# Optimization experiments

Hardware: AMD Instinct MI355X
Metric: run time of the kernel (lower is better)

Reference implementation:

```python
import jax, jax.numpy as jnp
import numpy as np

NUM_NODES_G1 = 60000
NUM_NODES_G2 = 50000
NUM_REL = 16
NUM_BASES = 4
DIM = 128  # node_dim == hidden_dim == final_dim
L_COMMON = 100


def _concept_layer(x, edge_index):
    # Gather-based concept propagation: x_i <- x_i + mean_{j in N(i)} x_j
    src, dst = edge_index[0], edge_index[1]
    n = x.shape[0]
    agg = jax.ops.segment_sum(x[src], dst, num_segments=n)
    deg = jax.ops.segment_sum(jnp.ones((src.shape[0],), x.dtype), dst, num_segments=n)
    return x + agg / jnp.clip(deg, 1.0)[:, None]


def _rgcn_layer(x, edge_index, edge_type, basis, comp, root, bias):
    # Basis-decomposed RGCN: out_i = x_i @ root + bias + sum_r (1/|N_i^r|) sum_{j in N_i^r} x_j @ W_r,
    # W_r = sum_b comp[r,b] * basis[b]. Reorder: scatter comp-weighted x[src] per basis, then one GEMM per basis.
    src, dst = edge_index[0], edge_index[1]
    n = x.shape[0]
    e = src.shape[0]
    seg = dst * NUM_REL + edge_type  # per-(node, relation) bucket
    cnt = jax.ops.segment_sum(jnp.ones((e,), x.dtype), seg, num_segments=n * NUM_REL)
    norm = 1.0 / jnp.clip(cnt, 1.0)
    coef = comp[edge_type] * norm[seg][:, None]  # [E, B]
    xsrc = x[src]  # [E, D] -- dominant gather traffic
    out = x @ root + bias
    for b in range(NUM_BASES):  # small fixed loop over bases
        agg_b = jax.ops.segment_sum(xsrc * coef[:, b:b + 1], dst, num_segments=n)
        out = out + agg_b @ basis[b]
    return out


def setup_inputs() -> dict:
    key = jax.random.key(0)
    ks = jax.random.split(key, 16)
    e2, e1 = 800000, 800000
    return {
        "edge_index_g2": jax.random.randint(ks[0], (2, e2), 0, NUM_NODES_G2),
        "edge_type_g2": jax.random.randint(ks[1], (e2,), 0, NUM_REL),
        "edge_index_g1": jax.random.randint(ks[2], (2, e1), 0, NUM_NODES_G1),
        "left_common": jax.random.randint(ks[3], (L_COMMON,), 0, NUM_NODES_G1),
        "all_node_embedding": jax.random.normal(ks[4], (NUM_NODES_G1, DIM), jnp.float32),
        "basis1": jax.random.normal(ks[5], (NUM_BASES, DIM, DIM), jnp.float32) * 0.05,
        "comp1": jax.random.normal(ks[6], (NUM_REL, NUM_BASES), jnp.float32),
        "root1": jax.random.normal(ks[7], (DIM, DIM), jnp.float32) * 0.05,
        "bias1": jnp.zeros((DIM,), jnp.float32),
        "basis2": jax.random.normal(ks[8], (NUM_BASES, DIM, DIM), jnp.float32) * 0.05,
        "comp2": jax.random.normal(ks[9], (NUM_REL, NUM_BASES), jnp.float32),
        "root2": jax.random.normal(ks[10], (DIM, DIM), jnp.float32) * 0.05,
        "bias2": jnp.zeros((DIM,), jnp.float32),
        "weights": jax.random.uniform(ks[11], (DIM, 1), jnp.float32),
    }


def reference(edge_index_g2, edge_type_g2, edge_index_g1, left_common,
              all_node_embedding, basis1, comp1, root1, bias1,
              basis2, comp2, root2, bias2, weights):
    x_g1 = jax.nn.relu(_concept_layer(all_node_embedding, edge_index_g1))
    x = x_g1[:NUM_NODES_G2]
    x = _rgcn_layer(x, edge_index_g2, edge_type_g2, basis1, comp1, root1, bias1)
    x = jax.nn.relu(x)  # relu_use == 1
    x_g2 = _rgcn_layer(x, edge_index_g2, edge_type_g2, basis2, comp2, root2, bias2)
    ty = x_g1[left_common]  # [L, D]
    # mul_def outer elementwise product followed by matmul with weights collapses to one contraction:
    # logits[n,l] = sum_d x_g2[n,d] * ty[l,d] * w[d]
    logits = jnp.einsum('nd,ld,d->nl', x_g2, ty, weights[:, 0])
    return jax.nn.softmax(logits, axis=1)
```

## Files before the change

kernel.cpp:

```cpp
#include <hip/hip_runtime.h>
#include <hip/hip_bf16.h>
#include <math.h>

#define N1 60000
#define N2 50000
#define DIM 128
#define NREL 16
#define NB 4
#define LCOM 100
#define LPAD 112

typedef __attribute__((ext_vector_type(8))) short short8;
typedef __attribute__((ext_vector_type(4))) float f32x4;

__device__ __forceinline__ float bf2f(unsigned short u) {
    union { unsigned int i; float f; } c; c.i = ((unsigned int)u) << 16; return c.f;
}
__device__ __forceinline__ unsigned short f2bf(float f) {
    union { float f; unsigned int i; } c; c.f = f;
    unsigned int r = c.i + 0x7FFF + ((c.i >> 16) & 1);
    return (unsigned short)(r >> 16);
}
__device__ __forceinline__ void split8(float4 a, float4 b, short8& h, short8& l) {
    float f[8] = {a.x, a.y, a.z, a.w, b.x, b.y, b.z, b.w};
#pragma unroll
    for (int j = 0; j < 8; j++) {
        unsigned short hh = f2bf(f[j]);
        h[j] = (short)hh;
        l[j] = (short)f2bf(f[j] - bf2f(hh));
    }
}

__global__ void k_prep_w(const float* __restrict__ root, const float* __restrict__ basis,
                         unsigned short* __restrict__ Wh, unsigned short* __restrict__ Wl) {
    int t = blockIdx.x * blockDim.x + threadIdx.x;
    if (t >= 640 * 128) return;
    int k = t >> 7, n = t & 127;
    float v = (k < 128) ? root[k * 128 + n] : basis[(k - 128) * 128 + n];
    unsigned short h = f2bf(v);
    Wh[n * 640 + k] = h;
    Wl[n * 640 + k] = f2bf(v - bf2f(h));
}

__global__ void k_hist_deg(const int* __restrict__ ei, int* __restrict__ deg, int E) {
    int e = blockIdx.x * blockDim.x + threadIdx.x;
    if (e >= E) return;
    atomicAdd(deg + ei[E + e], 1);
}

__global__ void k_hist_dt(const int* __restrict__ ei, const int* __restrict__ et,
                          int* __restrict__ cnt, int E) {
    int e = blockIdx.x * blockDim.x + threadIdx.x;
    if (e >= E) return;
    atomicAdd(cnt + ei[E + e] * NREL + et[e], 1);
}

__global__ void k_deg_from_cnt(const int* __restrict__ cnt, int* __restrict__ deg, int n) {
    int i = blockIdx.x * blockDim.x + threadIdx.x;
    if (i >= n) return;
    int s = 0;
#pragma unroll
    for (int t = 0; t < NREL; t++) s += cnt[i * NREL + t];
    deg[i] = s;
}

__global__ __launch_bounds__(256) void k_scan_p1(const int* __restrict__ in,
                                                 int* __restrict__ bsum, int n) {
    __shared__ int red[256];
    int base = blockIdx.x * 1024;
    int tid = threadIdx.x;
    int s = 0;
#pragma unroll
    for (int j = 0; j < 4; j++) {
        int i = base + tid * 4 + j;
        if (i < n) s += in[i];
    }
    red[tid] = s;
    __syncthreads();
    for (int d = 128; d; d >>= 1) {
        if (tid < d) red[tid] += red[tid + d];
        __syncthreads();
    }
    if (tid == 0) bsum[blockIdx.x] = red[0];
}

__global__ __launch_bounds__(64) void k_scan_p2(const int* __restrict__ bsum,
                                                int* __restrict__ boff,
                                                int* __restrict__ off, int nb, int n) {
    __shared__ int s[64];
    int tid = threadIdx.x;
    int v = (tid < nb) ? bsum[tid] : 0;
    s[tid] = v;
    __syncthreads();
    for (int d = 1; d < 64; d <<= 1) {
        int t = (tid >= d) ? s[tid - d] : 0;
        __syncthreads();
        s[tid] += t;
        __syncthreads();
    }
    if (tid < nb) boff[tid] = s[tid] - v;
    if (tid == 63) off[n] = s[63];
}

__global__ __launch_bounds__(256) void k_scan_p3(const int* __restrict__ in,
                                                 const int* __restrict__ boff,
                                                 int* __restrict__ off,
                                                 int* __restrict__ cur, int n) {
    __shared__ int red[256];
    int base = blockIdx.x * 1024;
    int tid = threadIdx.x;
    int v[4];
    int s = 0;
#pragma unroll
    for (int j = 0; j < 4; j++) {
        int i = base + tid * 4 + j;
        v[j] = (i < n) ? in[i] : 0;
        s += v[j];
    }
    red[tid] = s;
    __syncthreads();
    for (int d = 1; d < 256; d <<= 1) {
        int t = (tid >= d) ? red[tid - d] : 0;
        __syncthreads();
        red[tid] += t;
        __syncthreads();
    }
    int run = boff[blockIdx.x] + red[tid] - s;
#pragma unroll
    for (int j = 0; j < 4; j++) {
        int i = base + tid * 4 + j;
        if (i < n) {
            off[i] = run; cur[i] = run;
            run += v[j];
        }
    }
}

__global__ void k_csr_scatter1(const int* __restrict__ ei, int* __restrict__ cur,
                               int* __restrict__ elist, int E) {
    int e = blockIdx.x * blockDim.x + threadIdx.x;
    if (e >= E) return;
    int pos = atomicAdd(cur + ei[E + e], 1);
    elist[pos] = ei[e];
}

__global__ void k_csr_scatter2(const int* __restrict__ ei, const int* __restrict__ et,
                               const int* __restrict__ cnt, int* __restrict__ cur,
                               int* __restrict__ elist, float* __restrict__ nrmv, int E) {
    int e = blockIdx.x * blockDim.x + threadIdx.x;
    if (e >= E) return;
    int dst = ei[E + e], t = et[e];
    int pos = atomicAdd(cur + dst, 1);
    elist[pos] = (ei[e] << 4) | t;
    nrmv[pos] = 1.0f / fmaxf((float)cnt[dst * NREL + t], 1.0f);
}

__global__ __launch_bounds__(256) void k_concept_gather(const float* __restrict__ emb,
                                                        const int* __restrict__ off,
                                                        const int* __restrict__ elist,
                                                        float* __restrict__ xg1, int n) {
    int node = blockIdx.x * 4 + (threadIdx.x >> 6);
    int lane = threadIdx.x & 63;
    if (node >= n) return;
    int half = lane >> 5, d4 = (lane & 31) * 4;
    int s0 = off[node], s1 = off[node + 1];
    float4 acc = {0.f, 0.f, 0.f, 0.f};
    int i = s0;
    for (; i + 4 <= s1; i += 4) {
        int sa = elist[i + half];
        int sb = elist[i + 2 + half];
        float4 va = *(const float4*)(emb + (size_t)sa * DIM + d4);
        float4 vb = *(const float4*)(emb + (size_t)sb * DIM + d4);
        acc.x += va.x + vb.x; acc.y += va.y + vb.y;
        acc.z += va.z + vb.z; acc.w += va.w + vb.w;
    }
    for (; i < s1; i += 2) {
        int e = i + half;
        bool ok = e < s1;
        int s = elist[ok ? e : i];
        float4 v = *(const float4*)(emb + (size_t)s * DIM + d4);
        if (ok) { acc.x += v.x; acc.y += v.y; acc.z += v.z; acc.w += v.w; }
    }
    acc.x += __shfl_xor(acc.x, 32, 64);
    acc.y += __shfl_xor(acc.y, 32, 64);
    acc.z += __shfl_xor(acc.z, 32, 64);
    acc.w += __shfl_xor(acc.w, 32, 64);
    if (half == 0) {
        float inv = 1.0f / (float)max(s1 - s0, 1);
        float4 e = *(const float4*)(emb + (size_t)node * DIM + d4);
        float4 o = {fmaxf(e.x + acc.x * inv, 0.f), fmaxf(e.y + acc.y * inv, 0.f),
                    fmaxf(e.z + acc.z * inv, 0.f), fmaxf(e.w + acc.w * inv, 0.f)};
        *(float4*)(xg1 + (size_t)node * DIM + d4) = o;
    }
}

__global__ __launch_bounds__(64) void k_tyw(const float* __restrict__ emb,
                                            const int* __restrict__ off,
                                            const int* __restrict__ elist,
                                            const int* __restrict__ lc,
                                            const float* __restrict__ w,
                                            unsigned short* __restrict__ tyh,
                                            unsigned short* __restrict__ tyl) {
    int l = blockIdx.x;
    int lane = threadIdx.x;
    int d0 = lane * 2;
    if (l >= LCOM) {
        ushort2 z = {0, 0};
        *(ushort2*)(tyh + (size_t)l * 128 + d0) = z;
        *(ushort2*)(tyl + (size_t)l * 128 + d0) = z;
        return;
    }
    int row = lc[l];
    int s0 = off[row], s1 = off[row + 1];
    float2 acc = {0.f, 0.f};
    for (int i = s0; i < s1; i++) {
        int s = elist[i];
        float2 v = *(const float2*)(emb + (size_t)s * DIM + lane * 2);
        acc.x += v.x; acc.y += v.y;
    }
    float inv = 1.0f / (float)max(s1 - s0, 1);
    float2 e = *(const float2*)(emb + (size_t)row * DIM + lane * 2);
    float v0 = fmaxf(e.x + acc.x * inv, 0.f) * w[d0];
    float v1 = fmaxf(e.y + acc.y * inv, 0.f) * w[d0 + 1];
    unsigned short h0 = f2bf(v0), h1 = f2bf(v1);
    ushort2 hh = {h0, h1};
    ushort2 ll = {f2bf(v0 - bf2f(h0)), f2bf(v1 - bf2f(h1))};
    *(ushort2*)(tyh + (size_t)l * 128 + d0) = hh;
    *(ushort2*)(tyl + (size_t)l * 128 + d0) = ll;
}

__global__ __launch_bounds__(256) void k_rgcn_gather(const float* __restrict__ x,
                                                     const int* __restrict__ off,
                                                     const int* __restrict__ elist,
                                                     const float* __restrict__ nrmv,
                                                     const float* __restrict__ comp,
                                                     float* __restrict__ agg, int n) {
    __shared__ float scomp[NREL * NB];
    if (threadIdx.x < NREL * NB) scomp[threadIdx.x] = comp[threadIdx.x];
    __syncthreads();
    int node = blockIdx.x * 4 + (threadIdx.x >> 6);
    int lane = threadIdx.x & 63;
    if (node >= n) return;
    int half = lane >> 5, d4 = (lane & 31) * 4;
    int s0 = off[node], s1 = off[node + 1];
    float4 a0 = {0, 0, 0, 0}, a1 = a0, a2 = a0, a3 = a0;
    int i = s0;
#define RG_EDGE(E_IDX, NRM)                                                    \
    {                                                                          \
        int p = elist[E_IDX];                                                  \
        float nr = (NRM);                                                      \
        int s = p >> 4, t = p & 15;                                            \
        float4 cf = *(const float4*)(scomp + t * 4);                           \
        float4 v = *(const float4*)(x + (size_t)s * DIM + d4);                 \
        float c0 = cf.x * nr, c1 = cf.y * nr, c2 = cf.z * nr, c3 = cf.w * nr;  \
        a0.x = fmaf(c0, v.x, a0.x); a0.y = fmaf(c0, v.y, a0.y);                \
        a0.z = fmaf(c0, v.z, a0.z); a0.w = fmaf(c0, v.w, a0.w);                \
        a1.x = fmaf(c1, v.x, a1.x); a1.y = fmaf(c1, v.y, a1.y);                \
        a1.z = fmaf(c1, v.z, a1.z); a1.w = fmaf(c1, v.w, a1.w);                \
        a2.x = fmaf(c2, v.x, a2.x); a2.y = fmaf(c2, v.y, a2.y);                \
        a2.z = fmaf(c2, v.z, a2.z); a2.w = fmaf(c2, v.w, a2.w);                \
        a3.x = fmaf(c3, v.x, a3.x); a3.y = fmaf(c3, v.y, a3.y);                \
        a3.z = fmaf(c3, v.z, a3.z); a3.w = fmaf(c3, v.w, a3.w);                \
    }
    for (; i + 4 <= s1; i += 4) {
        RG_EDGE(i + half, nrmv[i + half]);
        RG_EDGE(i + 2 + half, nrmv[i + 2 + half]);
    }
    for (; i < s1; i += 2) {
        int e = i + half;
        bool ok = e < s1;
        int ei_ = ok ? e : i;
        RG_EDGE(ei_, ok ? nrmv[ei_] : 0.0f);
    }
#undef RG_EDGE
    a0.x += __shfl_xor(a0.x, 32, 64); a0.y += __shfl_xor(a0.y, 32, 64);
    a0.z += __shfl_xor(a0.z, 32, 64); a0.w += __shfl_xor(a0.w, 32, 64);
    a1.x += __shfl_xor(a1.x, 32, 64); a1.y += __shfl_xor(a1.y, 32, 64);
    a1.z += __shfl_xor(a1.z, 32, 64); a1.w += __shfl_xor(a1.w, 32, 64);
    a2.x += __shfl_xor(a2.x, 32, 64); a2.y += __shfl_xor(a2.y, 32, 64);
    a2.z += __shfl_xor(a2.z, 32, 64); a2.w += __shfl_xor(a2.w, 32, 64);
    a3.x += __shfl_xor(a3.x, 32, 64); a3.y += __shfl_xor(a3.y, 32, 64);
    a3.z += __shfl_xor(a3.z, 32, 64); a3.w += __shfl_xor(a3.w, 32, 64);
    if (half == 0) {
        float* o = agg + (size_t)node * (NB * DIM) + d4;
        *(float4*)(o + 0 * DIM) = a0;
        *(float4*)(o + 1 * DIM) = a1;
        *(float4*)(o + 2 * DIM) = a2;
        *(float4*)(o + 3 * DIM) = a3;
    }
}

#define LDSK 40
__global__ __launch_bounds__(256) void k_gemm(const float* __restrict__ x,
                                              const float* __restrict__ agg,
                                              const unsigned short* __restrict__ Wh,
                                              const unsigned short* __restrict__ Wl,
                                              const float* __restrict__ bias,
                                              float* __restrict__ out, int relu) {
    __shared__ __align__(16) short Ah[128 * LDSK];
    __shared__ __align__(16) short Al[128 * LDSK];
    __shared__ __align__(16) short Bh[128 * LDSK];
    __shared__ __align__(16) short Bl[128 * LDSK];
    int tid = threadIdx.x;
    int lane = tid & 63, wid = tid >> 6;
    int wave_m = wid >> 1, wave_n = wid & 1;
    int l15 = lane & 15, quad = lane >> 4;
    int row0 = blockIdx.x * 128;

    int srow = tid >> 1, skh = (tid & 1) * 16;

    f32x4 acc[4][4] = {};
    for (int k0 = 0; k0 < 640; k0 += 32) {
        {
            int rg = row0 + srow;
            float4 q0 = {0, 0, 0, 0}, q1 = q0, q2 = q0, q3 = q0;
            if (rg < N2) {
                const float* src = (k0 < 128) ? (x + (size_t)rg * 128 + k0 + skh)
                                              : (agg + (size_t)rg * 512 + (k0 - 128) + skh);
                q0 = *(const float4*)(src + 0);
                q1 = *(const float4*)(src + 4);
                q2 = *(const float4*)(src + 8);
                q3 = *(const float4*)(src + 12);
            }
            short8 h0, l0, h1, l1;
            split8(q0, q1, h0, l0);
            split8(q2, q3, h1, l1);
            *(short8*)(&Ah[srow * LDSK + skh]) = h0;
            *(short8*)(&Ah[srow * LDSK + skh + 8]) = h1;
            *(short8*)(&Al[srow * LDSK + skh]) = l0;
            *(short8*)(&Al[srow * LDSK + skh + 8]) = l1;
        }
        {
            const unsigned short* sh = Wh + (size_t)srow * 640 + k0 + skh;
            const unsigned short* sl = Wl + (size_t)srow * 640 + k0 + skh;
            *(short8*)(&Bh[srow * LDSK + skh]) = *(const short8*)(sh);
            *(short8*)(&Bh[srow * LDSK + skh + 8]) = *(const short8*)(sh + 8);
            *(short8*)(&Bl[srow * LDSK + skh]) = *(const short8*)(sl);
            *(short8*)(&Bl[srow * LDSK + skh + 8]) = *(const short8*)(sl + 8);
        }
        __syncthreads();
        short8 ah[4], al[4], bh[4], bl[4];
#pragma unroll
        for (int i = 0; i < 4; i++) {
            int ro = (wave_m * 64 + i * 16 + l15) * LDSK + quad * 8;
            ah[i] = *(const short8*)(&Ah[ro]);
            al[i] = *(const short8*)(&Al[ro]);
        }
#pragma unroll
        for (int j = 0; j < 4; j++) {
            int ro = (wave_n * 64 + j * 16 + l15) * LDSK + quad * 8;
            bh[j] = *(const short8*)(&Bh[ro]);
            bl[j] = *(const short8*)(&Bl[ro]);
        }
#pragma unroll
        for (int i = 0; i < 4; i++)
#pragma unroll
            for (int j = 0; j < 4; j++) {
                acc[i][j] = __builtin_amdgcn_mfma_f32_16x16x32_bf16(al[i], bh[j], acc[i][j], 0, 0, 0);
                acc[i][j] = __builtin_amdgcn_mfma_f32_16x16x32_bf16(ah[i], bl[j], acc[i][j], 0, 0, 0);
                acc[i][j] = __builtin_amdgcn_mfma_f32_16x16x32_bf16(ah[i], bh[j], acc[i][j], 0, 0, 0);
            }
        __syncthreads();
    }
#pragma unroll
    for (int j = 0; j < 4; j++) {
        int gcol = wave_n * 64 + j * 16 + l15;
        float bv = bias[gcol];
#pragma unroll
        for (int i = 0; i < 4; i++) {
            int grow_base = row0 + wave_m * 64 + i * 16 + quad * 4;
#pragma unroll
            for (int r = 0; r < 4; r++) {
                int grow = grow_base + r;
                if (grow >= N2) continue;
                float v = acc[i][j][r] + bv;
                if (relu) v = fmaxf(v, 0.f);
                out[(size_t)grow * 128 + gcol] = v;
            }
        }
    }
}

__global__ __launch_bounds__(256) void k_logits(const float* __restrict__ h2,
                                                const unsigned short* __restrict__ tyh,
                                                const unsigned short* __restrict__ tyl,
                                                float* __restrict__ out, int M) {
    int wid = threadIdx.x >> 6, lane = threadIdx.x & 63;
    int l15 = lane & 15, quad = lane >> 4;
    int row0w = blockIdx.x * 64 + wid * 16;
    int arow = min(row0w + l15, M - 1);
    f32x4 acc[7] = {};
#pragma unroll
    for (int k0 = 0; k0 < 128; k0 += 32) {
        const float* ap = h2 + (size_t)arow * 128 + k0 + quad * 8;
        float4 q0 = *(const float4*)(ap);
        float4 q1 = *(const float4*)(ap + 4);
        short8 ah, al;
        split8(q0, q1, ah, al);
#pragma unroll
        for (int j = 0; j < 7; j++) {
            size_t bo = (size_t)(j * 16 + l15) * 128 + k0 + quad * 8;
            short8 bh = *(const short8*)(tyh + bo);
            short8 bl = *(const short8*)(tyl + bo);
            acc[j] = __builtin_amdgcn_mfma_f32_16x16x32_bf16(al, bh, acc[j], 0, 0, 0);
            acc[j] = __builtin_amdgcn_mfma_f32_16x16x32_bf16(ah, bl, acc[j], 0, 0, 0);
            acc[j] = __builtin_amdgcn_mfma_f32_16x16x32_bf16(ah, bh, acc[j], 0, 0, 0);
        }
    }
    bool v6 = (l15 < LCOM - 96);
#pragma unroll
    for (int r = 0; r < 4; r++) {
        int grow = row0w + quad * 4 + r;
        float m = -INFINITY;
#pragma unroll
        for (int j = 0; j < 6; j++) m = fmaxf(m, acc[j][r]);
        if (v6) m = fmaxf(m, acc[6][r]);
        m = fmaxf(m, __shfl_xor(m, 8, 64));
        m = fmaxf(m, __shfl_xor(m, 4, 64));
        m = fmaxf(m, __shfl_xor(m, 2, 64));
        m = fmaxf(m, __shfl_xor(m, 1, 64));
        float e[7];
        float s = 0.f;
#pragma unroll
        for (int j = 0; j < 6; j++) { e[j] = __expf(acc[j][r] - m); s += e[j]; }
        e[6] = v6 ? __expf(acc[6][r] - m) : 0.f;
        s += e[6];
        s += __shfl_xor(s, 8, 64);
        s += __shfl_xor(s, 4, 64);
        s += __shfl_xor(s, 2, 64);
        s += __shfl_xor(s, 1, 64);
        float inv = 1.0f / s;
        if (grow < M) {
#pragma unroll
            for (int j = 0; j < 6; j++) out[(size_t)grow * LCOM + j * 16 + l15] = e[j] * inv;
            if (v6) out[(size_t)grow * LCOM + 96 + l15] = e[6] * inv;
        }
    }
}

extern "C" void kernel_launch(void* const* d_in, const int* in_sizes, int n_in,
                              void* d_out, int out_size, void* d_ws, size_t ws_size,
                              hipStream_t stream) {
    const int* ei2 = (const int*)d_in[0];
    const int* et2 = (const int*)d_in[1];
    const int* ei1 = (const int*)d_in[2];
    const int* lc = (const int*)d_in[3];
    const float* emb = (const float*)d_in[4];
    const float* basis1 = (const float*)d_in[5];
    const float* comp1 = (const float*)d_in[6];
    const float* root1 = (const float*)d_in[7];
    const float* bias1 = (const float*)d_in[8];
    const float* basis2 = (const float*)d_in[9];
    const float* comp2 = (const float*)d_in[10];
    const float* root2 = (const float*)d_in[11];
    const float* bias2 = (const float*)d_in[12];
    const float* wts = (const float*)d_in[13];
    float* out = (float*)d_out;
    int E2 = in_sizes[0] / 2, E1 = in_sizes[2] / 2;

    float* ws = (float*)d_ws;
    float* xg1 = ws;
    float* h1 = xg1 + 6400000;
    float* agg = h1 + 6400000;
    float* nrmv = agg + 25600000;
    unsigned short* tyh = (unsigned short*)(nrmv + 800000);
    unsigned short* tyl = tyh + LPAD * 128;
    unsigned short* Wh1 = tyl + LPAD * 128;
    unsigned short* Wl1 = Wh1 + 81920;
    unsigned short* Wh2 = Wl1 + 81920;
    unsigned short* Wl2 = Wh2 + 81920;
    int* ipool = (int*)(Wl2 + 81920);
    int* deg1 = ipool;
    int* off1 = deg1 + 60000;
    int* cur1 = off1 + 60001;
    int* elist1 = cur1 + 60000;
    int* cnt2 = elist1 + 800000;
    int* deg2 = cnt2 + 800000;
    int* off2 = deg2 + 50000;
    int* cur2 = off2 + 50001;
    int* elist2 = cur2 + 50000;
    int* bsum1 = elist2 + 800000;
    int* boff1 = bsum1 + 64;
    int* bsum2 = boff1 + 64;
    int* boff2 = bsum2 + 64;
    float* h2 = xg1;

    const int NB1 = (N1 + 1023) / 1024;
    const int NB2 = (N2 + 1023) / 1024;

    k_prep_w<<<(640 * 128 + 255) / 256, 256, 0, stream>>>(root1, basis1, Wh1, Wl1);
    k_prep_w<<<(640 * 128 + 255) / 256, 256, 0, stream>>>(root2, basis2, Wh2, Wl2);

    hipMemsetAsync(deg1, 0, 60000 * sizeof(int), stream);
    k_hist_deg<<<(E1 + 255) / 256, 256, 0, stream>>>(ei1, deg1, E1);
    k_scan_p1<<<NB1, 256, 0, stream>>>(deg1, bsum1, N1);
    k_scan_p2<<<1, 64, 0, stream>>>(bsum1, boff1, off1, NB1, N1);
    k_scan_p3<<<NB1, 256, 0, stream>>>(deg1, boff1, off1, cur1, N1);
    k_csr_scatter1<<<(E1 + 255) / 256, 256, 0, stream>>>(ei1, cur1, elist1, E1);
    k_concept_gather<<<(N2 + 3) / 4, 256, 0, stream>>>(emb, off1, elist1, xg1, N2);
    k_tyw<<<LPAD, 64, 0, stream>>>(emb, off1, elist1, lc, wts, tyh, tyl);

    hipMemsetAsync(cnt2, 0, 800000 * sizeof(int), stream);
    k_hist_dt<<<(E2 + 255) / 256, 256, 0, stream>>>(ei2, et2, cnt2, E2);
    k_deg_from_cnt<<<(N2 + 255) / 256, 256, 0, stream>>>(cnt2, deg2, N2);
    k_scan_p1<<<NB2, 256, 0, stream>>>(deg2, bsum2, N2);
    k_scan_p2<<<1, 64, 0, stream>>>(bsum2, boff2, off2, NB2, N2);
    k_scan_p3<<<NB2, 256, 0, stream>>>(deg2, boff2, off2, cur2, N2);
    k_csr_scatter2<<<(E2 + 255) / 256, 256, 0, stream>>>(ei2, et2, cnt2, cur2, elist2, nrmv, E2);

    k_rgcn_gather<<<(N2 + 3) / 4, 256, 0, stream>>>(xg1, off2, elist2, nrmv, comp1, agg, N2);
    k_gemm<<<(N2 + 127) / 128, 256, 0, stream>>>(xg1, agg, Wh1, Wl1, bias1, h1, 1);

    k_rgcn_gather<<<(N2 + 3) / 4, 256, 0, stream>>>(h1, off2, elist2, nrmv, comp2, agg, N2);
    k_gemm<<<(N2 + 127) / 128, 256, 0, stream>>>(h1, agg, Wh2, Wl2, bias2, h2, 0);

    k_logits<<<(N2 + 63) / 64, 256, 0, stream>>>(h2, tyh, tyl, out, N2);
}
```

Measured before the change: 629.2 us.

## Gather activations in fp16, merge graph-prep kernels, pack edge norms per node

The embedding and intermediate activations get fp16 shadow copies, written by a cast kernel and by the concept-gather and GEMM epilogues. Both RGCN gathers and the concept gather then read half-width rows, which targets the dominant random-gather bandwidth. The histogram, scan and CSR scatter kernels for both graphs are merged into shared launches. Per-relation counts are no longer built with atomics into a large array; instead each node counts its own relations in packed byte counters and writes (edge, norm) pairs together. This trades some precision in the gathered features, an fp16 rounding before fp32 accumulation, for less memory traffic and fewer launches.

```diff
diff --git a/kernel.cpp b/kernel.cpp
--- a/kernel.cpp
+++ b/kernel.cpp
@@ -12,6 +12,7 @@
 
 typedef __attribute__((ext_vector_type(8))) short short8;
 typedef __attribute__((ext_vector_type(4))) float f32x4;
+typedef __attribute__((ext_vector_type(4))) _Float16 half4;
 
 __device__ __forceinline__ float bf2f(unsigned short u) {
     union { unsigned int i; float f; } c; c.i = ((unsigned int)u) << 16; return c.f;
@@ -31,43 +32,49 @@
     }
 }
 
-__global__ void k_prep_w(const float* __restrict__ root, const float* __restrict__ basis,
-                         unsigned short* __restrict__ Wh, unsigned short* __restrict__ Wl) {
+__global__ void k_cast_emb(const float* __restrict__ emb, _Float16* __restrict__ embh, int n4) {
+    int i = blockIdx.x * blockDim.x + threadIdx.x;
+    if (i >= n4) return;
+    float4 v = ((const float4*)emb)[i];
+    half4 o = {(_Float16)v.x, (_Float16)v.y, (_Float16)v.z, (_Float16)v.w};
+    ((half4*)embh)[i] = o;
+}
+
+__global__ void k_prep_w2(const float* __restrict__ root1, const float* __restrict__ basis1,
+                          unsigned short* __restrict__ Wh1, unsigned short* __restrict__ Wl1,
+                          const float* __restrict__ root2, const float* __restrict__ basis2,
+                          unsigned short* __restrict__ Wh2, unsigned short* __restrict__ Wl2) {
     int t = blockIdx.x * blockDim.x + threadIdx.x;
-    if (t >= 640 * 128) return;
-    int k = t >> 7, n = t & 127;
+    if (t >= 2 * 640 * 128) return;
+    int which = t >= 640 * 128;
+    int tt = which ? t - 640 * 128 : t;
+    const float* root = which ? root2 : root1;
+    const float* basis = which ? basis2 : basis1;
+    unsigned short* Wh = which ? Wh2 : Wh1;
+    unsigned short* Wl = which ? Wl2 : Wl1;
+    int k = tt >> 7, n = tt & 127;
     float v = (k < 128) ? root[k * 128 + n] : basis[(k - 128) * 128 + n];
     unsigned short h = f2bf(v);
     Wh[n * 640 + k] = h;
     Wl[n * 640 + k] = f2bf(v - bf2f(h));
 }
 
-__global__ void k_hist_deg(const int* __restrict__ ei, int* __restrict__ deg, int E) {
-    int e = blockIdx.x * blockDim.x + threadIdx.x;
-    if (e >= E) return;
-    atomicAdd(deg + ei[E + e], 1);
-}
-
-__global__ void k_hist_dt(const int* __restrict__ ei, const int* __restrict__ et,
-                          int* __restrict__ cnt, int E) {
-    int e = blockIdx.x * blockDim.x + threadIdx.x;
-    if (e >= E) return;
-    atomicAdd(cnt + ei[E + e] * NREL + et[e], 1);
-}
-
-__global__ void k_deg_from_cnt(const int* __restrict__ cnt, int* __restrict__ deg, int n) {
-    int i = blockIdx.x * blockDim.x + threadIdx.x;
-    if (i >= n) return;
-    int s = 0;
-#pragma unroll
-    for (int t = 0; t < NREL; t++) s += cnt[i * NREL + t];
-    deg[i] = s;
-}
-
-__global__ __launch_bounds__(256) void k_scan_p1(const int* __restrict__ in,
-                                                 int* __restrict__ bsum, int n) {
+__global__ void k_hist_both(const int* __restrict__ ei1, int E1, int* __restrict__ deg1,
+                            const int* __restrict__ ei2, int E2, int* __restrict__ deg2) {
+    int g = blockIdx.x * blockDim.x + threadIdx.x;
+    if (g < E1) atomicAdd(deg1 + ei1[E1 + g], 1);
+    if (g < E2) atomicAdd(deg2 + ei2[E2 + g], 1);
+}
+
+__global__ __launch_bounds__(256) void k_scan_p1m(const int* __restrict__ inA, int nA, int nbA,
+                                                  int* __restrict__ bsumA,
+                                                  const int* __restrict__ inB, int nB,
+                                                  int* __restrict__ bsumB) {
     __shared__ int red[256];
-    int base = blockIdx.x * 1024;
+    const int* in; int n; int* bsum; int b;
+    if ((int)blockIdx.x < nbA) { in = inA; n = nA; bsum = bsumA; b = blockIdx.x; }
+    else { in = inB; n = nB; bsum = bsumB; b = blockIdx.x - nbA; }
+    int base = b * 1024;
     int tid = threadIdx.x;
     int s = 0;
 #pragma unroll
@@ -81,13 +88,17 @@
         if (tid < d) red[tid] += red[tid + d];
         __syncthreads();
     }
-    if (tid == 0) bsum[blockIdx.x] = red[0];
-}
-
-__global__ __launch_bounds__(64) void k_scan_p2(const int* __restrict__ bsum,
-                                                int* __restrict__ boff,
-                                                int* __restrict__ off, int nb, int n) {
+    if (tid == 0) bsum[b] = red[0];
+}
+
+__global__ __launch_bounds__(64) void k_scan_p2m(const int* __restrict__ bsumA, int* __restrict__ boffA,
+                                                 int* __restrict__ offA, int nbA, int nA,
+                                                 const int* __restrict__ bsumB, int* __restrict__ boffB,
+                                                 int* __restrict__ offB, int nbB, int nB) {
     __shared__ int s[64];
+    const int* bsum; int* boff; int* off; int nb; int n;
+    if (blockIdx.x == 0) { bsum = bsumA; boff = boffA; off = offA; nb = nbA; n = nA; }
+    else { bsum = bsumB; boff = boffB; off = offB; nb = nbB; n = nB; }
     int tid = threadIdx.x;
     int v = (tid < nb) ? bsum[tid] : 0;
     s[tid] = v;
@@ -102,12 +113,16 @@
     if (tid == 63) off[n] = s[63];
 }
 
-__global__ __launch_bounds__(256) void k_scan_p3(const int* __restrict__ in,
-                                                 const int* __restrict__ boff,
-                                                 int* __restrict__ off,
-                                                 int* __restrict__ cur, int n) {
+__global__ __launch_bounds__(256) void k_scan_p3m(const int* __restrict__ inA, const int* __restrict__ boffA,
+                                                  int* __restrict__ offA, int* __restrict__ curA,
+                                                  int nA, int nbA,
+                                                  const int* __restrict__ inB, const int* __restrict__ boffB,
+                                                  int* __restrict__ offB, int* __restrict__ curB, int nB) {
     __shared__ int red[256];
-    int base = blockIdx.x * 1024;
+    const int* in; const int* boff; int* off; int* cur; int n; int b;
+    if ((int)blockIdx.x < nbA) { in = inA; boff = boffA; off = offA; cur = curA; n = nA; b = blockIdx.x; }
+    else { in = inB; boff = boffB; off = offB; cur = curB; n = nB; b = blockIdx.x - nbA; }
+    int base = b * 1024;
     int tid = threadIdx.x;
     int v[4];
     int s = 0;
@@ -125,7 +140,7 @@
         red[tid] += t;
         __syncthreads();
     }
-    int run = boff[blockIdx.x] + red[tid] - s;
+    int run = boff[b] + red[tid] - s;
 #pragma unroll
     for (int j = 0; j < 4; j++) {
         int i = base + tid * 4 + j;
@@ -136,29 +151,50 @@
     }
 }
 
-__global__ void k_csr_scatter1(const int* __restrict__ ei, int* __restrict__ cur,
-                               int* __restrict__ elist, int E) {
-    int e = blockIdx.x * blockDim.x + threadIdx.x;
-    if (e >= E) return;
-    int pos = atomicAdd(cur + ei[E + e], 1);
-    elist[pos] = ei[e];
-}
-
-__global__ void k_csr_scatter2(const int* __restrict__ ei, const int* __restrict__ et,
-                               const int* __restrict__ cnt, int* __restrict__ cur,
-                               int* __restrict__ elist, float* __restrict__ nrmv, int E) {
-    int e = blockIdx.x * blockDim.x + threadIdx.x;
-    if (e >= E) return;
-    int dst = ei[E + e], t = et[e];
-    int pos = atomicAdd(cur + dst, 1);
-    elist[pos] = (ei[e] << 4) | t;
-    nrmv[pos] = 1.0f / fmaxf((float)cnt[dst * NREL + t], 1.0f);
-}
-
-__global__ __launch_bounds__(256) void k_concept_gather(const float* __restrict__ emb,
+__global__ void k_scat_both(const int* __restrict__ ei1, int E1, int* __restrict__ cur1,
+                            int* __restrict__ elist1,
+                            const int* __restrict__ ei2, const int* __restrict__ et2, int E2,
+                            int* __restrict__ cur2, int* __restrict__ elist2) {
+    int g = blockIdx.x * blockDim.x + threadIdx.x;
+    if (g < E1) {
+        int pos = atomicAdd(cur1 + ei1[E1 + g], 1);
+        elist1[pos] = ei1[g];
+    }
+    if (g < E2) {
+        int pos = atomicAdd(cur2 + ei2[E2 + g], 1);
+        elist2[pos] = (ei2[g] << 4) | et2[g];
+    }
+}
+
+__global__ void k_nrm_pack(const int* __restrict__ off, const int* __restrict__ elist,
+                           int2* __restrict__ epack, int n) {
+    int node = blockIdx.x * blockDim.x + threadIdx.x;
+    if (node >= n) return;
+    int s0 = off[node], s1 = off[node + 1];
+    unsigned long long c0 = 0, c1 = 0;
+    for (int i = s0; i < s1; i++) {
+        int t = elist[i] & 15;
+        if (t < 8) c0 += 1ull << (8 * t); else c1 += 1ull << (8 * (t - 8));
+    }
+    for (int i = s0; i < s1; i++) {
+        int p = elist[i];
+        int t = p & 15;
+        unsigned int c = (t < 8) ? (unsigned int)((c0 >> (8 * t)) & 255)
+                                 : (unsigned int)((c1 >> (8 * (t - 8))) & 255);
+        float nrm = 1.0f / (float)max(c, 1u);
+        int2 e;
+        e.x = p;
+        e.y = __float_as_int(nrm);
+        epack[i] = e;
+    }
+}
+
+__global__ __launch_bounds__(256) void k_concept_gather(const _Float16* __restrict__ embh,
+                                                        const float* __restrict__ emb,
                                                         const int* __restrict__ off,
                                                         const int* __restrict__ elist,
-                                                        float* __restrict__ xg1, int n) {
+                                                        float* __restrict__ xg1,
+                                                        _Float16* __restrict__ xg1h, int n) {
     int node = blockIdx.x * 4 + (threadIdx.x >> 6);
     int lane = threadIdx.x & 63;
     if (node >= n) return;
@@ -169,17 +205,22 @@
     for (; i + 4 <= s1; i += 4) {
         int sa = elist[i + half];
         int sb = elist[i + 2 + half];
-        float4 va = *(const float4*)(emb + (size_t)sa * DIM + d4);
-        float4 vb = *(const float4*)(emb + (size_t)sb * DIM + d4);
-        acc.x += va.x + vb.x; acc.y += va.y + vb.y;
-        acc.z += va.z + vb.z; acc.w += va.w + vb.w;
+        half4 ha = *(const half4*)(embh + (size_t)sa * DIM + d4);
+        half4 hb = *(const half4*)(embh + (size_t)sb * DIM + d4);
+        acc.x += (float)ha[0] + (float)hb[0];
+        acc.y += (float)ha[1] + (float)hb[1];
+        acc.z += (float)ha[2] + (float)hb[2];
+        acc.w += (float)ha[3] + (float)hb[3];
     }
     for (; i < s1; i += 2) {
         int e = i + half;
         bool ok = e < s1;
         int s = elist[ok ? e : i];
-        float4 v = *(const float4*)(emb + (size_t)s * DIM + d4);
-        if (ok) { acc.x += v.x; acc.y += v.y; acc.z += v.z; acc.w += v.w; }
+        half4 hv = *(const half4*)(embh + (size_t)s * DIM + d4);
+        if (ok) {
+            acc.x += (float)hv[0]; acc.y += (float)hv[1];
+            acc.z += (float)hv[2]; acc.w += (float)hv[3];
+        }
     }
     acc.x += __shfl_xor(acc.x, 32, 64);
     acc.y += __shfl_xor(acc.y, 32, 64);
@@ -191,6 +232,8 @@
         float4 o = {fmaxf(e.x + acc.x * inv, 0.f), fmaxf(e.y + acc.y * inv, 0.f),
                     fmaxf(e.z + acc.z * inv, 0.f), fmaxf(e.w + acc.w * inv, 0.f)};
         *(float4*)(xg1 + (size_t)node * DIM + d4) = o;
+        half4 oh = {(_Float16)o.x, (_Float16)o.y, (_Float16)o.z, (_Float16)o.w};
+        *(half4*)(xg1h + (size_t)node * DIM + d4) = oh;
     }
 }
 
@@ -229,10 +272,9 @@
     *(ushort2*)(tyl + (size_t)l * 128 + d0) = ll;
 }
 
-__global__ __launch_bounds__(256) void k_rgcn_gather(const float* __restrict__ x,
+__global__ __launch_bounds__(256) void k_rgcn_gather(const _Float16* __restrict__ xh,
                                                      const int* __restrict__ off,
-                                                     const int* __restrict__ elist,
-                                                     const float* __restrict__ nrmv,
+                                                     const int2* __restrict__ epack,
                                                      const float* __restrict__ comp,
                                                      float* __restrict__ agg, int n) {
     __shared__ float scomp[NREL * NB];
@@ -245,13 +287,14 @@
     int s0 = off[node], s1 = off[node + 1];
     float4 a0 = {0, 0, 0, 0}, a1 = a0, a2 = a0, a3 = a0;
     int i = s0;
-#define RG_EDGE(E_IDX, NRM)                                                    \
+#define RG_EDGE(E_IDX, GATE)                                                   \
     {                                                                          \
-        int p = elist[E_IDX];                                                  \
-        float nr = (NRM);                                                      \
-        int s = p >> 4, t = p & 15;                                            \
+        int2 pk = epack[E_IDX];                                                \
+        int s = pk.x >> 4, t = pk.x & 15;                                      \
+        float nr = __int_as_float(pk.y) * (GATE);                              \
         float4 cf = *(const float4*)(scomp + t * 4);                           \
-        float4 v = *(const float4*)(x + (size_t)s * DIM + d4);                 \
+        half4 hv = *(const half4*)(xh + (size_t)s * DIM + d4);                 \
+        float4 v = {(float)hv[0], (float)hv[1], (float)hv[2], (float)hv[3]};   \
         float c0 = cf.x * nr, c1 = cf.y * nr, c2 = cf.z * nr, c3 = cf.w * nr;  \
         a0.x = fmaf(c0, v.x, a0.x); a0.y = fmaf(c0, v.y, a0.y);                \
         a0.z = fmaf(c0, v.z, a0.z); a0.w = fmaf(c0, v.w, a0.w);                \
@@ -263,14 +306,14 @@
         a3.z = fmaf(c3, v.z, a3.z); a3.w = fmaf(c3, v.w, a3.w);                \
     }
     for (; i + 4 <= s1; i += 4) {
-        RG_EDGE(i + half, nrmv[i + half]);
-        RG_EDGE(i + 2 + half, nrmv[i + 2 + half]);
+        RG_EDGE(i + half, 1.0f);
+        RG_EDGE(i + 2 + half, 1.0f);
     }
     for (; i < s1; i += 2) {
         int e = i + half;
         bool ok = e < s1;
         int ei_ = ok ? e : i;
-        RG_EDGE(ei_, ok ? nrmv[ei_] : 0.0f);
+        RG_EDGE(ei_, ok ? 1.0f : 0.0f);
     }
 #undef RG_EDGE
     a0.x += __shfl_xor(a0.x, 32, 64); a0.y += __shfl_xor(a0.y, 32, 64);
@@ -296,7 +339,8 @@
                                               const unsigned short* __restrict__ Wh,
                                               const unsigned short* __restrict__ Wl,
                                               const float* __restrict__ bias,
-                                              float* __restrict__ out, int relu) {
+                                              float* __restrict__ out,
+                                              _Float16* __restrict__ out_h, int relu) {
     __shared__ __align__(16) short Ah[128 * LDSK];
     __shared__ __align__(16) short Al[128 * LDSK];
     __shared__ __align__(16) short Bh[128 * LDSK];
@@ -376,6 +420,7 @@
                 float v = acc[i][j][r] + bv;
                 if (relu) v = fmaxf(v, 0.f);
                 out[(size_t)grow * 128 + gcol] = v;
+                if (out_h) out_h[(size_t)grow * 128 + gcol] = (_Float16)v;
             }
         }
     }
@@ -462,8 +507,9 @@
     float* xg1 = ws;
     float* h1 = xg1 + 6400000;
     float* agg = h1 + 6400000;
-    float* nrmv = agg + 25600000;
-    unsigned short* tyh = (unsigned short*)(nrmv + 800000);
+    _Float16* emb_h = (_Float16*)(agg + 25600000);
+    int2* epack = (int2*)(emb_h + 7680000);
+    unsigned short* tyh = (unsigned short*)(epack + 800000);
     unsigned short* tyl = tyh + LPAD * 128;
     unsigned short* Wh1 = tyl + LPAD * 128;
     unsigned short* Wl1 = Wh1 + 81920;
@@ -471,48 +517,46 @@
     unsigned short* Wl2 = Wh2 + 81920;
     int* ipool = (int*)(Wl2 + 81920);
     int* deg1 = ipool;
-    int* off1 = deg1 + 60000;
+    int* deg2 = deg1 + 60000;
+    int* off1 = deg2 + 50000;
     int* cur1 = off1 + 60001;
     int* elist1 = cur1 + 60000;
-    int* cnt2 = elist1 + 800000;
-    int* deg2 = cnt2 + 800000;
-    int* off2 = deg2 + 50000;
+    int* off2 = elist1 + 800000;
     int* cur2 = off2 + 50001;
     int* elist2 = cur2 + 50000;
     int* bsum1 = elist2 + 800000;
     int* boff1 = bsum1 + 64;
     int* bsum2 = boff1 + 64;
     int* boff2 = bsum2 + 64;
+    _Float16* xg1_h = (_Float16*)h1;
+    _Float16* h1_h = emb_h;
     float* h2 = xg1;
 
     const int NB1 = (N1 + 1023) / 1024;
     const int NB2 = (N2 + 1023) / 1024;
 
-    k_prep_w<<<(640 * 128 + 255) / 256, 256, 0, stream>>>(root1, basis1, Wh1, Wl1);
-    k_prep_w<<<(640 * 128 + 255) / 256, 256, 0, stream>>>(root2, basis2, Wh2, Wl2);
-
-    hipMemsetAsync(deg1, 0, 60000 * sizeof(int), stream);
-    k_hist_deg<<<(E1 + 255) / 256, 256, 0, stream>>>(ei1, deg1, E1);
-    k_scan_p1<<<NB1, 256, 0, stream>>>(deg1, bsum1, N1);
-    k_scan_p2<<<1, 64, 0, stream>>>(bsum1, boff1, off1, NB1, N1);
-    k_scan_p3<<<NB1, 256, 0, stream>>>(deg1, boff1, off1, cur1, N1);
-    k_csr_scatter1<<<(E1 + 255) / 256, 256, 0, stream>>>(ei1, cur1, elist1, E1);
-    k_concept_gather<<<(N2 + 3) / 4, 256, 0, stream>>>(emb, off1, elist1, xg1, N2);
+    k_prep_w2<<<(2 * 640 * 128 + 255) / 256, 256, 0, stream>>>(root1, basis1, Wh1, Wl1,
+                                                               root2, basis2, Wh2, Wl2);
+    k_cast_emb<<<(N1 * DIM / 4 + 255) / 256, 256, 0, stream>>>(emb, emb_h, N1 * DIM / 4);
+    hipMemsetAsync(deg1, 0, (60000 + 50000) * sizeof(int), stream);
+
+    k_hist_both<<<(max(E1, E2) + 255) / 256, 256, 0, stream>>>(ei1, E1, deg1, ei2, E2, deg2);
+    k_scan_p1m<<<NB1 + NB2, 256, 0, stream>>>(deg1, N1, NB1, bsum1, deg2, N2, bsum2);
+    k_scan_p2m<<<2, 64, 0, stream>>>(bsum1, boff1, off1, NB1, N1, bsum2, boff2, off2, NB2, N2);
+    k_scan_p3m<<<NB1 + NB2, 256, 0, stream>>>(deg1, boff1, off1, cur1, N1, NB1,
+                                              deg2, boff2, off2, cur2, N2);
+    k_scat_both<<<(max(E1, E2) + 255) / 256, 256, 0, stream>>>(ei1, E1, cur1, elist1,
+                                                               ei2, et2, E2, cur2, elist2);
+    k_nrm_pack<<<(N2 + 255) / 256, 256, 0, stream>>>(off2, elist2, epack, N2);
+
+    k_concept_gather<<<(N2 + 3) / 4, 256, 0, stream>>>(emb_h, emb, off1, elist1, xg1, xg1_h, N2);
     k_tyw<<<LPAD, 64, 0, stream>>>(emb, off1, elist1, lc, wts, tyh, tyl);
 
-    hipMemsetAsync(cnt2, 0, 800000 * sizeof(int), stream);
-    k_hist_dt<<<(E2 + 255) / 256, 256, 0, stream>>>(ei2, et2, cnt2, E2);
-    k_deg_from_cnt<<<(N2 + 255) / 256, 256, 0, stream>>>(cnt2, deg2, N2);
-    k_scan_p1<<<NB2, 256, 0, stream>>>(deg2, bsum2, N2);
-    k_scan_p2<<<1, 64, 0, stream>>>(bsum2, boff2, off2, NB2, N2);
-    k_scan_p3<<<NB2, 256, 0, stream>>>(deg2, boff2, off2, cur2, N2);
-    k_csr_scatter2<<<(E2 + 255) / 256, 256, 0, stream>>>(ei2, et2, cnt2, cur2, elist2, nrmv, E2);
-
-    k_rgcn_gather<<<(N2 + 3) / 4, 256, 0, stream>>>(xg1, off2, elist2, nrmv, comp1, agg, N2);
-    k_gemm<<<(N2 + 127) / 128, 256, 0, stream>>>(xg1, agg, Wh1, Wl1, bias1, h1, 1);
-
-    k_rgcn_gather<<<(N2 + 3) / 4, 256, 0, stream>>>(h1, off2, elist2, nrmv, comp2, agg, N2);
-    k_gemm<<<(N2 + 127) / 128, 256, 0, stream>>>(h1, agg, Wh2, Wl2, bias2, h2, 0);
+    k_rgcn_gather<<<(N2 + 3) / 4, 256, 0, stream>>>(xg1_h, off2, epack, comp1, agg, N2);
+    k_gemm<<<(N2 + 127) / 128, 256, 0, stream>>>(xg1, agg, Wh1, Wl1, bias1, h1, h1_h, 1);
+
+    k_rgcn_gather<<<(N2 + 3) / 4, 256, 0, stream>>>(h1_h, off2, epack, comp2, agg, N2);
+    k_gemm<<<(N2 + 127) / 128, 256, 0, stream>>>(h1, agg, Wh2, Wl2, bias2, h2, (_Float16*)nullptr, 0);
 
     k_logits<<<(N2 + 63) / 64, 256, 0, stream>>>(h2, tyh, tyl, out, N2);
 }
```

After: 597.4 us. 1.05x faster.
